# Optimization experiments

Hardware: AMD Instinct MI355X
Metric: run time of the kernel (lower is better)

Reference implementation:

```python
import jax, jax.numpy as jnp
import numpy as np

N = 50000
E = 800000
IN_CH = 512
OUT_CH = 64
ITERATIONS = 3  # adjacency power order; iterations-1 spmm steps


def setup_inputs() -> dict:
    key = jax.random.key(0)
    k1, k2, k3, k4, k5 = jax.random.split(key, 5)
    adj_indices = jax.random.randint(k1, (2, E), 0, N, dtype=jnp.int32)
    adj_values = jax.random.uniform(k2, (E,), dtype=jnp.float32)
    features = jax.random.normal(k3, (N, IN_CH), dtype=jnp.float32)
    # xavier-uniform init bounds
    bw = float(np.sqrt(6.0 / (IN_CH + OUT_CH)))
    weight = jax.random.uniform(k4, (IN_CH, OUT_CH), minval=-bw, maxval=bw, dtype=jnp.float32)
    bb = float(np.sqrt(6.0 / (1 + OUT_CH)))
    bias = jax.random.uniform(k5, (1, OUT_CH), minval=-bb, maxval=bb, dtype=jnp.float32)
    return {"adj_indices": adj_indices, "adj_values": adj_values,
            "features": features, "weight": weight, "bias": bias}


def reference(adj_indices, adj_values, features, weight, bias):
    # dense projection: [N, in] @ [in, out] -> [N, out]
    x = features @ weight
    # dropout is identity in eval mode (training=False)
    row, col = adj_indices[0], adj_indices[1]
    # (iterations - 1) sparse-dense matmuls: x <- A @ x
    for _ in range(ITERATIONS - 1):
        gathered = adj_values[:, None] * x[col]          # [E, out]
        x = jax.ops.segment_sum(gathered, row, num_segments=N)
    return x + bias
```

## Files before the change

### kernel.cpp

```cpp
#include <hip/hip_runtime.h>
#include <hip/hip_bf16.h>
#include <hip/hip_fp16.h>

#define NN 50000
#define INCH 512
#define OUTCH 64
#define NTILES 3125
#define MAXD 48
#define DEGSTR 16
#define GB 782
#define SB 1024

typedef __attribute__((ext_vector_type(8))) short short8;
typedef __attribute__((ext_vector_type(4))) float floatx4;

__device__ __forceinline__ unsigned packbf2(float a, float b) {
    __hip_bfloat162 h = __float22bfloat162_rn(make_float2(a, b));
    unsigned r;
    __builtin_memcpy(&r, &h, 4);
    return r;
}
__device__ __forceinline__ unsigned short f2bf(float f) {
    unsigned u = __float_as_uint(f);
    return (unsigned short)((u + 0x7FFFu + ((u >> 16) & 1u)) >> 16);
}
__device__ __forceinline__ float bf2f(unsigned short u) {
    return __uint_as_float(((unsigned)u) << 16);
}

__global__ __launch_bounds__(256) void prep_kernel(const float* __restrict__ W,
                                                   unsigned short* __restrict__ Wbf,
                                                   int* __restrict__ deg) {
    const int i = blockIdx.x * 256 + threadIdx.x;
    if (i < (NN * DEGSTR) / 4)
        *reinterpret_cast<uint4*>(deg + i * 4) = uint4{0u, 0u, 0u, 0u};
    if (i < INCH * OUTCH) {
        const int k = i >> 6;
        const int n = i & 63;
        Wbf[n * INCH + k] = f2bf(W[i]);
    }
}

__global__ __launch_bounds__(256, 4) void fused_gemm_scatter(
        const float* __restrict__ A, const unsigned short* __restrict__ Wbf,
        unsigned short* __restrict__ C,
        const int* __restrict__ rows, const int* __restrict__ cols,
        const float* __restrict__ vals, int* __restrict__ deg,
        unsigned* __restrict__ ell, int E_) {
    __shared__ unsigned short ldsT[4][16 * 64];
    const int t = threadIdx.x;

    if (blockIdx.x >= GB) {
        for (int e = (blockIdx.x - GB) * 256 + t; e < E_; e += SB * 256) {
            const int r = rows[e];
            const int c = cols[e];
            const float v = vals[e];
            const int slot = atomicAdd(&deg[r * DEGSTR], 1);
            const unsigned short hv = __half_as_ushort(__float2half(v));
            if (slot < MAXD)
                ell[(size_t)r * MAXD + slot] = (unsigned)c | ((unsigned)hv << 16);
        }
        return;
    }

    const int lane = t & 63;
    const int wave = t >> 6;
    const int tile = blockIdx.x * 4 + wave;
    if (tile >= NTILES) return;
    const int rbase = tile * 16;
    const int frow = lane & 15;
    const int quad = lane >> 4;
    const float* Ap = A + (size_t)(rbase + frow) * INCH + quad * 8;
    const unsigned short* Bp = Wbf + frow * INCH + quad * 8;

    floatx4 acc[4] = {floatx4{0,0,0,0}, floatx4{0,0,0,0}, floatx4{0,0,0,0}, floatx4{0,0,0,0}};

#pragma unroll
    for (int c = 0; c < 16; ++c) {
        const float4 a0 = *(const float4*)(Ap + c * 32);
        const float4 a1 = *(const float4*)(Ap + c * 32 + 4);
        short8 bfr[4];
#pragma unroll
        for (int f = 0; f < 4; ++f)
            bfr[f] = *(const short8*)(Bp + (size_t)f * 16 * INCH + c * 32);
        uint4 au;
        au.x = packbf2(a0.x, a0.y);
        au.y = packbf2(a0.z, a0.w);
        au.z = packbf2(a1.x, a1.y);
        au.w = packbf2(a1.z, a1.w);
        const short8 af = *(const short8*)&au;
#pragma unroll
        for (int f = 0; f < 4; ++f)
            acc[f] = __builtin_amdgcn_mfma_f32_16x16x32_bf16(af, bfr[f], acc[f], 0, 0, 0);
    }

    unsigned short* myT = ldsT[wave];
#pragma unroll
    for (int f = 0; f < 4; ++f)
#pragma unroll
        for (int reg = 0; reg < 4; ++reg)
            myT[(quad * 4 + reg) * 64 + f * 16 + frow] = f2bf(acc[f][reg]);
    unsigned short* Cw = C + (size_t)rbase * OUTCH;
#pragma unroll
    for (int it = 0; it < 2; ++it) {
        const short8 v = *(const short8*)&myT[it * 512 + lane * 8];
        *(short8*)(Cw + it * 512 + lane * 8) = v;
    }
}

template <bool LAST>
__global__ __launch_bounds__(256) void spmm_ell(const int* __restrict__ deg,
                                                const unsigned* __restrict__ ell,
                                                const unsigned short* __restrict__ xin,
                                                void* __restrict__ xout_,
                                                const float* __restrict__ bias) {
    const int b = blockIdx.x;
    const int xcd = b & 7;
    const int half = xcd >> 2;
    const int rowgrp = (b >> 3) * 4 + (xcd & 3);
    const int t = threadIdx.x;
    const int lane = t & 63;
    const int eslot = lane >> 2;
    const int cg = lane & 3;
    const int row = rowgrp * 4 + (t >> 6);
    int d = deg[row * DEGSTR];
    d = d < MAXD ? d : MAXD;
    const unsigned* ebase = ell + (size_t)row * MAXD;

    unsigned p0 = ebase[eslot];
    unsigned p1 = ebase[eslot + 16];
    unsigned p2 = ebase[eslot + 32];
    if (eslot >= d)      p0 = 0u;
    if (eslot + 16 >= d) p1 = 0u;
    if (eslot + 32 >= d) p2 = 0u;

    const unsigned short* xh = xin + half * 32 + cg * 8;
    float acc[8] = {0.f, 0.f, 0.f, 0.f, 0.f, 0.f, 0.f, 0.f};

    auto gath = [&](unsigned P) {
        const short8 xv = *(const short8*)(xh + (size_t)(P & 0xFFFFu) * OUTCH);
        const float v = __half2float(__ushort_as_half((unsigned short)(P >> 16)));
#pragma unroll
        for (int j = 0; j < 8; ++j)
            acc[j] = fmaf(v, bf2f((unsigned short)xv[j]), acc[j]);
    };
    if (d > 0)  gath(p0);
    if (d > 16) gath(p1);
    if (d > 32) gath(p2);

#pragma unroll
    for (int j = 0; j < 8; ++j) {
        acc[j] += __shfl_xor(acc[j], 4, 64);
        acc[j] += __shfl_xor(acc[j], 8, 64);
        acc[j] += __shfl_xor(acc[j], 16, 64);
        acc[j] += __shfl_xor(acc[j], 32, 64);
    }

    if (eslot == 0) {
        const int chb = half * 32 + cg * 8;
        if (LAST) {
            float* op = (float*)xout_ + (size_t)row * OUTCH + chb;
            const float4 b0 = *(const float4*)(bias + chb);
            const float4 b1 = *(const float4*)(bias + chb + 4);
            float4 o0, o1;
            o0.x = acc[0] + b0.x; o0.y = acc[1] + b0.y;
            o0.z = acc[2] + b0.z; o0.w = acc[3] + b0.w;
            o1.x = acc[4] + b1.x; o1.y = acc[5] + b1.y;
            o1.z = acc[6] + b1.z; o1.w = acc[7] + b1.w;
            *(float4*)op = o0;
            *(float4*)(op + 4) = o1;
        } else {
            unsigned short* op = (unsigned short*)xout_ + (size_t)row * OUTCH + chb;
            short8 o;
#pragma unroll
            for (int j = 0; j < 8; ++j) o[j] = (short)f2bf(acc[j]);
            *(short8*)op = o;
        }
    }
}

extern "C" void kernel_launch(void* const* d_in, const int* in_sizes, int n_in,
                              void* d_out, int out_size, void* d_ws, size_t ws_size,
                              hipStream_t stream) {
    const int*   adj   = (const int*)d_in[0];
    const float* avals = (const float*)d_in[1];
    const float* feat  = (const float*)d_in[2];
    const float* W     = (const float*)d_in[3];
    const float* bias  = (const float*)d_in[4];
    float* out = (float*)d_out;

    const int E_ = in_sizes[1];
    const int* rows = adj;
    const int* cols = adj + E_;

    unsigned short* x0  = (unsigned short*)d_ws;
    unsigned short* x1  = x0 + (size_t)NN * OUTCH;
    unsigned short* Wbf = x1 + (size_t)NN * OUTCH;
    unsigned* ell = (unsigned*)(Wbf + (size_t)OUTCH * INCH);
    int* deg = (int*)(ell + (size_t)NN * MAXD);

    prep_kernel<<<(NN * DEGSTR / 4 + 255) / 256, 256, 0, stream>>>(W, Wbf, deg);

    fused_gemm_scatter<<<GB + SB, 256, 0, stream>>>(feat, Wbf, x0, rows, cols, avals,
                                                    deg, ell, E_);

    spmm_ell<false><<<3125 * 8, 256, 0, stream>>>(deg, ell, x0, x1, nullptr);
    spmm_ell<true><<<3125 * 8, 256, 0, stream>>>(deg, ell, x1, out, bias);
}
```

Measured before the change: 282.2 us.

## Split feature matrix into 16-channel quarter planes and partition atomics by XCD

The intermediate bf16 feature matrices are stored as four 16-channel planes instead of row-major 64 channels. Each XCD (chosen by block index mod 8) gathers from only one quarter plane, so its working set in that XCD's L2 shrinks. The SpMM grid doubles to 50000 blocks, each handling 4 channels per lane. Separately, the ELL-building scatter blocks now each scan a slice of the edges and only do the atomics for rows whose index mod 8 matches their XCD, to keep atomic traffic local to one XCD. The cost is that every edge is read by eight blocks, SpMM launches twice as many blocks, and each lane does narrower gathers.

```diff
diff --git a/kernel.cpp b/kernel.cpp
--- a/kernel.cpp
+++ b/kernel.cpp
@@ -51,14 +51,18 @@
     const int t = threadIdx.x;
 
     if (blockIdx.x >= GB) {
-        for (int e = (blockIdx.x - GB) * 256 + t; e < E_; e += SB * 256) {
+        const int xcd = blockIdx.x & 7;
+        const int rank = (blockIdx.x - GB) >> 3;
+        for (int e = rank * 256 + t; e < E_; e += (SB / 8) * 256) {
             const int r = rows[e];
             const int c = cols[e];
             const float v = vals[e];
-            const int slot = atomicAdd(&deg[r * DEGSTR], 1);
-            const unsigned short hv = __half_as_ushort(__float2half(v));
-            if (slot < MAXD)
-                ell[(size_t)r * MAXD + slot] = (unsigned)c | ((unsigned)hv << 16);
+            if ((r & 7) == xcd) {
+                const int slot = atomicAdd(&deg[r * DEGSTR], 1);
+                const unsigned short hv = __half_as_ushort(__float2half(v));
+                if (slot < MAXD)
+                    ell[(size_t)r * MAXD + slot] = (unsigned)c | ((unsigned)hv << 16);
+            }
         }
         return;
     }
@@ -100,11 +104,13 @@
 #pragma unroll
         for (int reg = 0; reg < 4; ++reg)
             myT[(quad * 4 + reg) * 64 + f * 16 + frow] = f2bf(acc[f][reg]);
-    unsigned short* Cw = C + (size_t)rbase * OUTCH;
-#pragma unroll
-    for (int it = 0; it < 2; ++it) {
-        const short8 v = *(const short8*)&myT[it * 512 + lane * 8];
-        *(short8*)(Cw + it * 512 + lane * 8) = v;
+    {
+        const int q = lane >> 4;
+        const int sub = lane & 15;
+        unsigned short* dst = C + (size_t)q * NN * 16 + (size_t)(rbase + sub) * 16;
+        const unsigned short* src = myT + sub * 64 + q * 16;
+        *(short8*)dst = *(const short8*)src;
+        *(short8*)(dst + 8) = *(const short8*)(src + 8);
     }
 }
 
@@ -116,8 +122,9 @@
                                                 const float* __restrict__ bias) {
     const int b = blockIdx.x;
     const int xcd = b & 7;
-    const int half = xcd >> 2;
-    const int rowgrp = (b >> 3) * 4 + (xcd & 3);
+    const int q = xcd >> 1;
+    const int p = xcd & 1;
+    const int rowgrp = (b >> 3) * 2 + p;
     const int t = threadIdx.x;
     const int lane = t & 63;
     const int eslot = lane >> 2;
@@ -134,47 +141,43 @@
     if (eslot + 16 >= d) p1 = 0u;
     if (eslot + 32 >= d) p2 = 0u;
 
-    const unsigned short* xh = xin + half * 32 + cg * 8;
-    float acc[8] = {0.f, 0.f, 0.f, 0.f, 0.f, 0.f, 0.f, 0.f};
+    const unsigned short* xq = xin + (size_t)q * NN * 16 + cg * 4;
+    float a0 = 0.f, a1 = 0.f, a2 = 0.f, a3 = 0.f;
 
     auto gath = [&](unsigned P) {
-        const short8 xv = *(const short8*)(xh + (size_t)(P & 0xFFFFu) * OUTCH);
+        const ushort4 xv = *(const ushort4*)(xq + (size_t)(P & 0xFFFFu) * 16);
         const float v = __half2float(__ushort_as_half((unsigned short)(P >> 16)));
-#pragma unroll
-        for (int j = 0; j < 8; ++j)
-            acc[j] = fmaf(v, bf2f((unsigned short)xv[j]), acc[j]);
+        a0 = fmaf(v, bf2f(xv.x), a0);
+        a1 = fmaf(v, bf2f(xv.y), a1);
+        a2 = fmaf(v, bf2f(xv.z), a2);
+        a3 = fmaf(v, bf2f(xv.w), a3);
     };
     if (d > 0)  gath(p0);
     if (d > 16) gath(p1);
     if (d > 32) gath(p2);
 
-#pragma unroll
-    for (int j = 0; j < 8; ++j) {
-        acc[j] += __shfl_xor(acc[j], 4, 64);
-        acc[j] += __shfl_xor(acc[j], 8, 64);
-        acc[j] += __shfl_xor(acc[j], 16, 64);
-        acc[j] += __shfl_xor(acc[j], 32, 64);
-    }
+    a0 += __shfl_xor(a0, 4, 64);  a1 += __shfl_xor(a1, 4, 64);
+    a2 += __shfl_xor(a2, 4, 64);  a3 += __shfl_xor(a3, 4, 64);
+    a0 += __shfl_xor(a0, 8, 64);  a1 += __shfl_xor(a1, 8, 64);
+    a2 += __shfl_xor(a2, 8, 64);  a3 += __shfl_xor(a3, 8, 64);
+    a0 += __shfl_xor(a0, 16, 64); a1 += __shfl_xor(a1, 16, 64);
+    a2 += __shfl_xor(a2, 16, 64); a3 += __shfl_xor(a3, 16, 64);
+    a0 += __shfl_xor(a0, 32, 64); a1 += __shfl_xor(a1, 32, 64);
+    a2 += __shfl_xor(a2, 32, 64); a3 += __shfl_xor(a3, 32, 64);
 
     if (eslot == 0) {
-        const int chb = half * 32 + cg * 8;
         if (LAST) {
-            float* op = (float*)xout_ + (size_t)row * OUTCH + chb;
-            const float4 b0 = *(const float4*)(bias + chb);
-            const float4 b1 = *(const float4*)(bias + chb + 4);
-            float4 o0, o1;
-            o0.x = acc[0] + b0.x; o0.y = acc[1] + b0.y;
-            o0.z = acc[2] + b0.z; o0.w = acc[3] + b0.w;
-            o1.x = acc[4] + b1.x; o1.y = acc[5] + b1.y;
-            o1.z = acc[6] + b1.z; o1.w = acc[7] + b1.w;
-            *(float4*)op = o0;
-            *(float4*)(op + 4) = o1;
+            const int chb = q * 16 + cg * 4;
+            const float4 bv = *(const float4*)(bias + chb);
+            float4 o;
+            o.x = a0 + bv.x; o.y = a1 + bv.y; o.z = a2 + bv.z; o.w = a3 + bv.w;
+            *(float4*)((float*)xout_ + (size_t)row * OUTCH + chb) = o;
         } else {
-            unsigned short* op = (unsigned short*)xout_ + (size_t)row * OUTCH + chb;
-            short8 o;
-#pragma unroll
-            for (int j = 0; j < 8; ++j) o[j] = (short)f2bf(acc[j]);
-            *(short8*)op = o;
+            unsigned short* op = (unsigned short*)xout_ + (size_t)q * NN * 16
+                               + (size_t)row * 16 + cg * 4;
+            ushort4 o;
+            o.x = f2bf(a0); o.y = f2bf(a1); o.z = f2bf(a2); o.w = f2bf(a3);
+            *(ushort4*)op = o;
         }
     }
 }
@@ -204,6 +207,6 @@
     fused_gemm_scatter<<<GB + SB, 256, 0, stream>>>(feat, Wbf, x0, rows, cols, avals,
                                                     deg, ell, E_);
 
-    spmm_ell<false><<<3125 * 8, 256, 0, stream>>>(deg, ell, x0, x1, nullptr);
-    spmm_ell<true><<<3125 * 8, 256, 0, stream>>>(deg, ell, x1, out, bias);
-}
+    spmm_ell<false><<<50000, 256, 0, stream>>>(deg, ell, x0, x1, nullptr);
+    spmm_ell<true><<<50000, 256, 0, stream>>>(deg, ell, x1, out, bias);
+}
```

New measurement: 322.2 us. 14.2% more time.
